# Kernel tuning notes

Measured on AMD Instinct MI355X. Metric: run time of the kernel, lower is better.

Reference implementation:

```python
import jax, jax.numpy as jnp
import numpy as np

D_MODEL = 512
N_HEAD = 8
D_K = 64
EPS = 1e-5


def setup_inputs() -> dict:
    key = jax.random.key(0)
    ks = jax.random.split(key, 12)
    B, S = 4, 2048
    Q = jax.random.normal(ks[0], (B, S, D_MODEL), dtype=jnp.float32)
    K = jax.random.normal(ks[1], (B, S, D_MODEL), dtype=jnp.float32)
    V = jax.random.normal(ks[2], (B, S, D_MODEL), dtype=jnp.float32)
    # bool padding-style mask: True = masked position
    att_mask = jax.random.randint(ks[3], (B, S, S), 0, 2).astype(bool)
    s = 1.0 / np.sqrt(D_MODEL)
    # Linear weights stored as [in, out] (transpose of torch's [out, in]; same math)
    Wq = jax.random.uniform(ks[4], (D_MODEL, N_HEAD * D_K), jnp.float32, -s, s)
    bq = jax.random.uniform(ks[5], (N_HEAD * D_K,), jnp.float32, -s, s)
    Wk = jax.random.uniform(ks[6], (D_MODEL, N_HEAD * D_K), jnp.float32, -s, s)
    bk = jax.random.uniform(ks[7], (N_HEAD * D_K,), jnp.float32, -s, s)
    Wv = jax.random.uniform(ks[8], (D_MODEL, N_HEAD * D_K), jnp.float32, -s, s)
    bv = jax.random.uniform(ks[9], (N_HEAD * D_K,), jnp.float32, -s, s)
    Wo = jax.random.uniform(ks[10], (N_HEAD * D_K, D_MODEL), jnp.float32, -s, s)
    bo = jax.random.uniform(ks[11], (D_MODEL,), jnp.float32, -s, s)
    return {"Q": Q, "K": K, "V": V, "att_mask": att_mask,
            "Wq": Wq, "bq": bq, "Wk": Wk, "bk": bk,
            "Wv": Wv, "bv": bv, "Wo": Wo, "bo": bo}


def _layer_norm(x):
    # nn.LayerNorm with default weight=1, bias=0 (fresh module in forward)
    mu = jnp.mean(x, axis=-1, keepdims=True)
    var = jnp.mean(jnp.square(x - mu), axis=-1, keepdims=True)
    return (x - mu) / jnp.sqrt(var + EPS)


def reference(Q, K, V, att_mask, Wq, bq, Wk, bk, Wv, bv, Wo, bo):
    B, S, _ = Q.shape
    residual = Q
    # QKV projections -> [B, H, S, Dk]
    q = (Q @ Wq + bq).reshape(B, S, N_HEAD, D_K).transpose(0, 2, 1, 3)
    k = (K @ Wk + bk).reshape(B, S, N_HEAD, D_K).transpose(0, 2, 1, 3)
    v = (V @ Wv + bv).reshape(B, S, N_HEAD, D_K).transpose(0, 2, 1, 3)
    # scaled dot-product attention with padding mask
    score = jnp.einsum('bhqd,bhkd->bhqk', q, k) / np.sqrt(D_K)
    score = jnp.where(att_mask[:, None, :, :], jnp.float32(-1e9), score)
    attn = jax.nn.softmax(score, axis=-1)
    context = jnp.einsum('bhqk,bhkd->bhqd', attn, v)
    context = context.transpose(0, 2, 1, 3).reshape(B, S, N_HEAD * D_K)
    output = context @ Wo + bo
    out = _layer_norm(output + residual)
    return out, attn
```

## Files before the change

### kernel.cpp

```cpp
#include <hip/hip_runtime.h>
#include <hip/hip_bf16.h>
#include <cstdint>
#include <cstddef>


typedef __attribute__((ext_vector_type(8)))  short short8v;
typedef __attribute__((ext_vector_type(2)))  float f32x2;
typedef __attribute__((ext_vector_type(4)))  float f32x4;
typedef __attribute__((ext_vector_type(16))) float f32x16;

constexpr int DM = 512, S = 2048, BATCH = 4, NHEAD = 8, DK = 64;
constexpr int ROWS = BATCH * S;
constexpr int BH   = BATCH * NHEAD;
constexpr size_t OUT_ELEMS = (size_t)ROWS * DM;
constexpr size_t HFRAG = 131072;

#define ZERO16 {0.f,0.f,0.f,0.f,0.f,0.f,0.f,0.f,0.f,0.f,0.f,0.f,0.f,0.f,0.f,0.f}

__device__ __forceinline__ unsigned short f2bf(float f) {
    union { __hip_bfloat16 b; unsigned short u; } c;
    c.b = __float2bfloat16(f);
    return c.u;
}
__device__ __forceinline__ float bf2f(unsigned short u) {
    union { float f; unsigned u32; } c;
    c.u32 = (unsigned)u << 16;
    return c.f;
}

__global__ __launch_bounds__(256)
void wconv(const float* __restrict__ Wq, const float* __restrict__ Wk,
           const float* __restrict__ Wv, const float* __restrict__ Wo,
           unsigned short* __restrict__ wt)
{
    __shared__ float T[32][33];
    const float* srcs[4] = {Wq, Wk, Wv, Wo};
    const float* W = srcs[blockIdx.z];
    unsigned short* out = wt + (size_t)blockIdx.z * DM * DM;
    const int r0 = blockIdx.y * 32, c0 = blockIdx.x * 32;
    const int tid = threadIdx.x;
#pragma unroll
    for (int i = 0; i < 4; ++i) {
        int lin = tid + i * 256; int r = lin >> 5, c = lin & 31;
        T[r][c] = W[(size_t)(r0 + r) * DM + c0 + c];
    }
    __syncthreads();
#pragma unroll
    for (int i = 0; i < 4; ++i) {
        int lin = tid + i * 256; int rn = lin >> 5, ck = lin & 31;
        out[(size_t)(c0 + rn) * DM + r0 + ck] = f2bf(T[ck][rn]);
    }
}

__global__ __launch_bounds__(256)
void maskpack(const uint8_t* __restrict__ mask, unsigned* __restrict__ mb)
{
    const int t = threadIdx.x;
    const int row = blockIdx.x * 4 + (t >> 6);
    const int w = t & 63;
    const uint8_t* src = mask + (size_t)row * S + 32 * w;
    const uint4 a = *reinterpret_cast<const uint4*>(src);
    const uint4 b = *reinterpret_cast<const uint4*>(src + 16);
    const unsigned m8[8] = {a.x, a.y, a.z, a.w, b.x, b.y, b.z, b.w};
    unsigned bits = 0;
#pragma unroll
    for (int k2 = 0; k2 < 32; ++k2)
        bits |= (((m8[k2 >> 2] >> (8 * (k2 & 3))) & 0xffu) ? 1u : 0u) << k2;
    mb[(size_t)row * 64 + w] = bits;
}

__global__ __launch_bounds__(256)
void proj3_mfma(const float* __restrict__ Qin, const float* __restrict__ Kin,
                const float* __restrict__ Vin, const unsigned short* __restrict__ wt,
                const float* __restrict__ bq, const float* __restrict__ bk,
                const float* __restrict__ bv,
                unsigned short* __restrict__ qo, unsigned short* __restrict__ ko,
                unsigned short* __restrict__ vo)
{
    const int z = blockIdx.z;
    const float* X = (z == 0) ? Qin : (z == 1) ? Kin : Vin;
    const unsigned short* Wt = wt + (size_t)z * DM * DM;
    const float* bias = (z == 0) ? bq : (z == 1) ? bk : bv;
    unsigned short* Y = (z == 0) ? qo : (z == 1) ? ko : vo;
    const float scale = (z == 0) ? 0.125f : 1.0f;

    const int tid = threadIdx.x, wv = tid >> 6, l = tid & 63, lr = l & 31, lh = l >> 5;
    const int m0 = blockIdx.y * 128 + wv * 32;
    const int n0 = blockIdx.x * 64;
    const float* xp = X + (size_t)(m0 + lr) * DM + 8 * lh;
    const unsigned short* w0 = Wt + (size_t)(n0 + lr) * DM + 8 * lh;
    const unsigned short* w1 = w0 + (size_t)32 * DM;
    f32x16 acc0 = ZERO16, acc1 = ZERO16;
#pragma unroll 8
    for (int t = 0; t < 32; ++t) {
        float4 xa = *reinterpret_cast<const float4*>(xp + 16 * t);
        float4 xb = *reinterpret_cast<const float4*>(xp + 16 * t + 4);
        short8v a;
        a[0] = (short)f2bf(xa.x * scale); a[1] = (short)f2bf(xa.y * scale);
        a[2] = (short)f2bf(xa.z * scale); a[3] = (short)f2bf(xa.w * scale);
        a[4] = (short)f2bf(xb.x * scale); a[5] = (short)f2bf(xb.y * scale);
        a[6] = (short)f2bf(xb.z * scale); a[7] = (short)f2bf(xb.w * scale);
        short8v b0 = *reinterpret_cast<const short8v*>(w0 + 16 * t);
        short8v b1 = *reinterpret_cast<const short8v*>(w1 + 16 * t);
        acc0 = __builtin_amdgcn_mfma_f32_32x32x16_bf16(a, b0, acc0, 0, 0, 0);
        acc1 = __builtin_amdgcn_mfma_f32_32x32x16_bf16(a, b1, acc1, 0, 0, 0);
    }
#pragma unroll
    for (int j = 0; j < 2; ++j) {
        const f32x16 acc = j ? acc1 : acc0;
        const int n = n0 + 32 * j + lr;
        const float bvv = bias[n] * scale;
        const int h = n >> 6, d = n & 63;
#pragma unroll
        for (int r = 0; r < 16; ++r) {
            const int m = m0 + (r & 3) + 8 * (r >> 2) + 4 * lh;
            const int bb = m >> 11, s = m & (S - 1);
            const int bh = bb * NHEAD + h;
            const unsigned short val = f2bf(acc[r] + bvv);
            size_t idx;
            if (z == 0)
                idx = ((size_t)bh * S + s) * DK + d;
            else if (z == 1)
                idx = (size_t)bh * HFRAG + (size_t)(s >> 4) * 1024 + (size_t)(d >> 5) * 512
                      + (size_t)(((s & 15) + 16 * ((d & 31) >> 3)) << 3) + (d & 7);
            else
                idx = (size_t)bh * HFRAG + (size_t)(s >> 5) * 2048 + (size_t)(d >> 4) * 512
                      + (size_t)(((d & 15) + 16 * ((s & 31) >> 3)) << 3) + (s & 7);
            Y[idx] = val;
        }
    }
}

__global__ __launch_bounds__(512, 4)
void attn_fused(const unsigned short* __restrict__ q,
                const unsigned short* __restrict__ kpack,
                const unsigned short* __restrict__ vpack,
                const unsigned* __restrict__ mbits,
                float* __restrict__ attn,
                unsigned short* __restrict__ ctx)
{
    __shared__ char Pc[16 * 4096];
    __shared__ float cred[2][4][16][16];
    __shared__ float redm[8][16];
    __shared__ float reds[8][16];
    const int tid = threadIdx.x, wv = tid >> 6, l = tid & 63;
    const int lq = l & 15, lg = l >> 4;
    const int bh = blockIdx.y, q0 = blockIdx.x * 16;
    const int b = bh >> 3, h = bh & 7;

    const unsigned short* qp = q + ((size_t)bh * S + q0 + lq) * DK + 8 * lg;
    const short8v qf0 = *reinterpret_cast<const short8v*>(qp);
    const short8v qf1 = *reinterpret_cast<const short8v*>(qp + 32);
    const unsigned short* kbase = kpack + (size_t)bh * HFRAG + (size_t)l * 8;
    f32x4 acc[16];
#pragma unroll
    for (int it = 0; it < 16; ++it) {
        const unsigned short* kc = kbase + (size_t)(16 * wv + it) * 1024;
        const short8v kf0 = *reinterpret_cast<const short8v*>(kc);
        const short8v kf1 = *reinterpret_cast<const short8v*>(kc + 512);
        f32x4 a = {0.f, 0.f, 0.f, 0.f};
        a = __builtin_amdgcn_mfma_f32_16x16x32_bf16(kf0, qf0, a, 0, 0, 0);
        a = __builtin_amdgcn_mfma_f32_16x16x32_bf16(kf1, qf1, a, 0, 0, 0);
        acc[it] = a;
    }

    const unsigned* mrow = mbits + ((size_t)b * S + q0 + lq) * 64 + 8 * wv;
    const uint4 mwa = *reinterpret_cast<const uint4*>(mrow);
    const uint4 mwb = *reinterpret_cast<const uint4*>(mrow + 4);
    const unsigned mw[8] = {mwa.x, mwa.y, mwa.z, mwa.w, mwb.x, mwb.y, mwb.z, mwb.w};
    float vmax = -3e38f;
#pragma unroll
    for (int it = 0; it < 16; ++it) {
        const unsigned word = mw[it >> 1] >> (16 * (it & 1) + 4 * lg);
#pragma unroll
        for (int r = 0; r < 4; ++r) {
            const float v = ((word >> r) & 1u) ? -1e30f : acc[it][r];
            acc[it][r] = v;
            vmax = fmaxf(vmax, v);
        }
    }
    vmax = fmaxf(vmax, __shfl_xor(vmax, 16));
    vmax = fmaxf(vmax, __shfl_xor(vmax, 32));
    if (l < 16) redm[wv][l] = vmax;
    __syncthreads();
    float rmax = redm[0][lq];
#pragma unroll
    for (int w2 = 1; w2 < 8; ++w2) rmax = fmaxf(rmax, redm[w2][lq]);

    float sum = 0.f;
#pragma unroll
    for (int it = 0; it < 16; ++it)
#pragma unroll
        for (int r = 0; r < 4; ++r) {
            const float v = __expf(acc[it][r] - rmax);
            acc[it][r] = v;
            sum += v;
        }
    sum += __shfl_xor(sum, 16);
    sum += __shfl_xor(sum, 32);
    if (l < 16) reds[wv][l] = sum;
    __syncthreads();
    float rsum = 0.f;
#pragma unroll
    for (int w2 = 0; w2 < 8; ++w2) rsum += reds[w2][lq];
    const float inv = 1.0f / rsum;

    float* arow = attn + ((size_t)bh * S + q0 + lq) * S + 256 * wv;
    const int swz = (lq & 7) << 4;
    char* prow = Pc + lq * 4096;
#pragma unroll
    for (int it = 0; it < 16; ++it) {
        const int n = 16 * it + 4 * lg;
        f32x4 o;
        o[0] = acc[it][0] * inv; o[1] = acc[it][1] * inv;
        o[2] = acc[it][2] * inv; o[3] = acc[it][3] * inv;
        __builtin_nontemporal_store(o, reinterpret_cast<f32x4*>(arow + n));
        ushort4 p;
        p.x = f2bf(o[0]); p.y = f2bf(o[1]); p.z = f2bf(o[2]); p.w = f2bf(o[3]);
        *reinterpret_cast<ushort4*>(prow + ((2 * (256 * wv + n)) ^ swz)) = p;
    }
    __syncthreads();

    const int dt = wv & 3, kh = wv >> 2;
    const int rswz = (lq & 7) << 4;
    f32x4 pacc = {0.f, 0.f, 0.f, 0.f};
    const unsigned short* vbase = vpack + (size_t)bh * HFRAG + dt * 512 + (size_t)l * 8;
#pragma unroll 4
    for (int s = 0; s < 32; ++s) {
        const int kk0 = kh * 1024 + 32 * s;
        const short8v a = *reinterpret_cast<const short8v*>(
            Pc + lq * 4096 + ((2 * (kk0 + 8 * lg)) ^ rswz));
        const short8v bf = *reinterpret_cast<const short8v*>(
            vbase + (size_t)(kh * 32 + s) * 2048);
        pacc = __builtin_amdgcn_mfma_f32_16x16x32_bf16(a, bf, pacc, 0, 0, 0);
    }
#pragma unroll
    for (int r = 0; r < 4; ++r) cred[kh][dt][lg * 4 + r][lq] = pacc[r];
    __syncthreads();

    for (int o = tid; o < 1024; o += 512) {
        const int qq = o >> 6, dd = o & 63;
        const float val = cred[0][dd >> 4][qq][dd & 15] + cred[1][dd >> 4][qq][dd & 15];
        ctx[((size_t)(b * S + q0 + qq)) * DM + h * DK + dd] = f2bf(val);
    }
}

__global__ __launch_bounds__(512)
void out_ln(const unsigned short* __restrict__ Xc, const unsigned short* __restrict__ Wt,
            const float* __restrict__ bias, const float* __restrict__ resid,
            float* __restrict__ out)
{
    __shared__ f32x2 red[32][8];
    __shared__ f32x2 stat[32];
    const int tid = threadIdx.x, wv = tid >> 6, l = tid & 63, lr = l & 31, lh = l >> 5;
    const int m0 = blockIdx.x * 32;
    const int n0 = wv * 64;
    const unsigned short* xp = Xc + (size_t)(m0 + lr) * DM + 8 * lh;
    const unsigned short* w0 = Wt + (size_t)(n0 + lr) * DM + 8 * lh;
    const unsigned short* w1 = w0 + (size_t)32 * DM;
    f32x16 acc0 = ZERO16, acc1 = ZERO16;
#pragma unroll 8
    for (int t = 0; t < 32; ++t) {
        short8v a  = *reinterpret_cast<const short8v*>(xp + 16 * t);
        short8v b0 = *reinterpret_cast<const short8v*>(w0 + 16 * t);
        short8v b1 = *reinterpret_cast<const short8v*>(w1 + 16 * t);
        acc0 = __builtin_amdgcn_mfma_f32_32x32x16_bf16(a, b0, acc0, 0, 0, 0);
        acc1 = __builtin_amdgcn_mfma_f32_32x32x16_bf16(a, b1, acc1, 0, 0, 0);
    }
    const float bv0 = bias[n0 + lr], bv1 = bias[n0 + 32 + lr];
#pragma unroll
    for (int r = 0; r < 16; ++r) {
        const int mloc = (r & 3) + 8 * (r >> 2) + 4 * lh;
        const size_t mbase = (size_t)(m0 + mloc) * DM + n0 + lr;
        const float v0 = acc0[r] + bv0 + resid[mbase];
        const float v1 = acc1[r] + bv1 + resid[mbase + 32];
        acc0[r] = v0; acc1[r] = v1;
        float s = v0 + v1, sq = v0 * v0 + v1 * v1;
#pragma unroll
        for (int off = 16; off; off >>= 1) {
            s  += __shfl_xor(s, off);
            sq += __shfl_xor(sq, off);
        }
        if (lr == 0) { f32x2 t2; t2[0] = s; t2[1] = sq; red[mloc][wv] = t2; }
    }
    __syncthreads();
    if (tid < 32) {
        float s = 0.f, sq = 0.f;
#pragma unroll
        for (int w2 = 0; w2 < 8; ++w2) { s += red[tid][w2][0]; sq += red[tid][w2][1]; }
        const float mean = s * (1.0f / 512.0f);
        const float var = sq * (1.0f / 512.0f) - mean * mean;
        f32x2 t2; t2[0] = mean; t2[1] = rsqrtf(var + 1e-5f);
        stat[tid] = t2;
    }
    __syncthreads();
#pragma unroll
    for (int r = 0; r < 16; ++r) {
        const int mloc = (r & 3) + 8 * (r >> 2) + 4 * lh;
        const f32x2 st = stat[mloc];
        const size_t mbase = (size_t)(m0 + mloc) * DM + n0 + lr;
        out[mbase]      = (acc0[r] - st[0]) * st[1];
        out[mbase + 32] = (acc1[r] - st[0]) * st[1];
    }
}

extern "C" void kernel_launch(void* const* d_in, const int* in_sizes, int n_in,
                              void* d_out, int out_size, void* d_ws, size_t ws_size,
                              hipStream_t stream)
{
    (void)in_sizes; (void)n_in; (void)out_size; (void)ws_size;

    const float*   Qin  = (const float*)d_in[0];
    const float*   Kin  = (const float*)d_in[1];
    const float*   Vin  = (const float*)d_in[2];
    const uint8_t* mask = (const uint8_t*)d_in[3];
    const float*   Wq   = (const float*)d_in[4];
    const float*   bq   = (const float*)d_in[5];
    const float*   Wk   = (const float*)d_in[6];
    const float*   bk   = (const float*)d_in[7];
    const float*   Wv   = (const float*)d_in[8];
    const float*   bv   = (const float*)d_in[9];
    const float*   Wo   = (const float*)d_in[10];
    const float*   bo   = (const float*)d_in[11];

    float* out  = (float*)d_out;
    float* attn = out + OUT_ELEMS;

    char* w = (char*)d_ws;
    const size_t MB = 1 << 20;
    unsigned short* wt    = (unsigned short*)(w);
    unsigned short* qbf   = (unsigned short*)(w + 2  * MB);
    unsigned short* kpack = (unsigned short*)(w + 10 * MB);
    unsigned short* vpack = (unsigned short*)(w + 18 * MB);
    unsigned short* ctx   = (unsigned short*)(w + 26 * MB);
    unsigned*       mbits = (unsigned*)(w + 34 * MB);

    unsigned short* wto = wt + 3 * (size_t)DM * DM;

    wconv<<<dim3(16, 16, 4), 256, 0, stream>>>(Wq, Wk, Wv, Wo, wt);

    maskpack<<<ROWS / 4, 256, 0, stream>>>(mask, mbits);

    proj3_mfma<<<dim3(DM / 64, ROWS / 128, 3), 256, 0, stream>>>(
        Qin, Kin, Vin, wt, bq, bk, bv, qbf, kpack, vpack);

    attn_fused<<<dim3(S / 16, BH), 512, 0, stream>>>(qbf, kpack, vpack, mbits, attn, ctx);

    out_ln<<<ROWS / 32, 512, 0, stream>>>(ctx, wto, bo, Qin, out);
}
```

Baseline: 365.1 us.

## Make attention blocks loop over query tiles and overlap attn stores with MFMA

The attention kernel now launches a fixed grid of 512 blocks. Each block walks 8 query tiles of one head instead of handling a single tile. The fp32 attention-probability writes are no longer issued in one burst after the softmax. They are re-read from the bf16 P tile in shared memory and interleaved with the QK MFMAs of the next tile and the first PV MFMAs, so the heavy global write traffic overlaps with compute. In exchange the stored attn values are now bf16-rounded rather than full fp32, and the smaller grid lowers resident blocks per CU.

```diff
diff --git a/kernel.cpp b/kernel.cpp
--- a/kernel.cpp
+++ b/kernel.cpp
@@ -14,6 +14,7 @@
 constexpr int BH   = BATCH * NHEAD;
 constexpr size_t OUT_ELEMS = (size_t)ROWS * DM;
 constexpr size_t HFRAG = 131072;
+constexpr int TPB_TILES = 8;
 
 #define ZERO16 {0.f,0.f,0.f,0.f,0.f,0.f,0.f,0.f,0.f,0.f,0.f,0.f,0.f,0.f,0.f,0.f}
 
@@ -145,104 +146,142 @@
     __shared__ float reds[8][16];
     const int tid = threadIdx.x, wv = tid >> 6, l = tid & 63;
     const int lq = l & 15, lg = l >> 4;
-    const int bh = blockIdx.y, q0 = blockIdx.x * 16;
+    const int bid = blockIdx.x;
+    const int bh = bid & 31, slot = bid >> 5;
     const int b = bh >> 3, h = bh & 7;
 
-    const unsigned short* qp = q + ((size_t)bh * S + q0 + lq) * DK + 8 * lg;
-    const short8v qf0 = *reinterpret_cast<const short8v*>(qp);
-    const short8v qf1 = *reinterpret_cast<const short8v*>(qp + 32);
     const unsigned short* kbase = kpack + (size_t)bh * HFRAG + (size_t)l * 8;
-    f32x4 acc[16];
-#pragma unroll
-    for (int it = 0; it < 16; ++it) {
-        const unsigned short* kc = kbase + (size_t)(16 * wv + it) * 1024;
-        const short8v kf0 = *reinterpret_cast<const short8v*>(kc);
-        const short8v kf1 = *reinterpret_cast<const short8v*>(kc + 512);
-        f32x4 a = {0.f, 0.f, 0.f, 0.f};
-        a = __builtin_amdgcn_mfma_f32_16x16x32_bf16(kf0, qf0, a, 0, 0, 0);
-        a = __builtin_amdgcn_mfma_f32_16x16x32_bf16(kf1, qf1, a, 0, 0, 0);
-        acc[it] = a;
-    }
-
-    const unsigned* mrow = mbits + ((size_t)b * S + q0 + lq) * 64 + 8 * wv;
-    const uint4 mwa = *reinterpret_cast<const uint4*>(mrow);
-    const uint4 mwb = *reinterpret_cast<const uint4*>(mrow + 4);
-    const unsigned mw[8] = {mwa.x, mwa.y, mwa.z, mwa.w, mwb.x, mwb.y, mwb.z, mwb.w};
-    float vmax = -3e38f;
-#pragma unroll
-    for (int it = 0; it < 16; ++it) {
-        const unsigned word = mw[it >> 1] >> (16 * (it & 1) + 4 * lg);
-#pragma unroll
-        for (int r = 0; r < 4; ++r) {
-            const float v = ((word >> r) & 1u) ? -1e30f : acc[it][r];
-            acc[it][r] = v;
-            vmax = fmaxf(vmax, v);
-        }
-    }
-    vmax = fmaxf(vmax, __shfl_xor(vmax, 16));
-    vmax = fmaxf(vmax, __shfl_xor(vmax, 32));
-    if (l < 16) redm[wv][l] = vmax;
-    __syncthreads();
-    float rmax = redm[0][lq];
-#pragma unroll
-    for (int w2 = 1; w2 < 8; ++w2) rmax = fmaxf(rmax, redm[w2][lq]);
-
-    float sum = 0.f;
-#pragma unroll
-    for (int it = 0; it < 16; ++it)
-#pragma unroll
-        for (int r = 0; r < 4; ++r) {
-            const float v = __expf(acc[it][r] - rmax);
-            acc[it][r] = v;
-            sum += v;
-        }
-    sum += __shfl_xor(sum, 16);
-    sum += __shfl_xor(sum, 32);
-    if (l < 16) reds[wv][l] = sum;
-    __syncthreads();
-    float rsum = 0.f;
-#pragma unroll
-    for (int w2 = 0; w2 < 8; ++w2) rsum += reds[w2][lq];
-    const float inv = 1.0f / rsum;
-
-    float* arow = attn + ((size_t)bh * S + q0 + lq) * S + 256 * wv;
-    const int swz = (lq & 7) << 4;
-    char* prow = Pc + lq * 4096;
-#pragma unroll
-    for (int it = 0; it < 16; ++it) {
-        const int n = 16 * it + 4 * lg;
-        f32x4 o;
-        o[0] = acc[it][0] * inv; o[1] = acc[it][1] * inv;
-        o[2] = acc[it][2] * inv; o[3] = acc[it][3] * inv;
-        __builtin_nontemporal_store(o, reinterpret_cast<f32x4*>(arow + n));
-        ushort4 p;
-        p.x = f2bf(o[0]); p.y = f2bf(o[1]); p.z = f2bf(o[2]); p.w = f2bf(o[3]);
-        *reinterpret_cast<ushort4*>(prow + ((2 * (256 * wv + n)) ^ swz)) = p;
-    }
-    __syncthreads();
-
     const int dt = wv & 3, kh = wv >> 2;
+    const unsigned short* vbase = vpack + (size_t)bh * HFRAG + dt * 512 + (size_t)l * 8;
     const int rswz = (lq & 7) << 4;
-    f32x4 pacc = {0.f, 0.f, 0.f, 0.f};
-    const unsigned short* vbase = vpack + (size_t)bh * HFRAG + dt * 512 + (size_t)l * 8;
-#pragma unroll 4
-    for (int s = 0; s < 32; ++s) {
-        const int kk0 = kh * 1024 + 32 * s;
-        const short8v a = *reinterpret_cast<const short8v*>(
-            Pc + lq * 4096 + ((2 * (kk0 + 8 * lg)) ^ rswz));
-        const short8v bf = *reinterpret_cast<const short8v*>(
-            vbase + (size_t)(kh * 32 + s) * 2048);
-        pacc = __builtin_amdgcn_mfma_f32_16x16x32_bf16(a, bf, pacc, 0, 0, 0);
-    }
-#pragma unroll
-    for (int r = 0; r < 4; ++r) cred[kh][dt][lg * 4 + r][lq] = pacc[r];
-    __syncthreads();
-
-    for (int o = tid; o < 1024; o += 512) {
-        const int qq = o >> 6, dd = o & 63;
-        const float val = cred[0][dd >> 4][qq][dd & 15] + cred[1][dd >> 4][qq][dd & 15];
-        ctx[((size_t)(b * S + q0 + qq)) * DM + h * DK + dd] = f2bf(val);
-    }
+
+    const int srow = 2 * wv + (l >> 5);
+    const int sswz = (srow & 7) << 4;
+    const int scol = 4 * (l & 31);
+    auto store_attn = [&](float* sb, int c) {
+        const uint2 pw = *reinterpret_cast<const uint2*>(
+            Pc + srow * 4096 + ((2 * c) ^ sswz));
+        f32x4 st;
+        st[0] = bf2f((unsigned short)(pw.x & 0xffffu));
+        st[1] = bf2f((unsigned short)(pw.x >> 16));
+        st[2] = bf2f((unsigned short)(pw.y & 0xffffu));
+        st[3] = bf2f((unsigned short)(pw.y >> 16));
+        __builtin_nontemporal_store(st, reinterpret_cast<f32x4*>(sb + c));
+    };
+
+    int q0p = -1;
+    for (int t = 0; t < TPB_TILES; ++t) {
+        const int q0 = (slot + 16 * t) * 16;
+
+        const unsigned short* qp = q + ((size_t)bh * S + q0 + lq) * DK + 8 * lg;
+        const short8v qf0 = *reinterpret_cast<const short8v*>(qp);
+        const short8v qf1 = *reinterpret_cast<const short8v*>(qp + 32);
+        float* sbp = (q0p >= 0)
+            ? attn + ((size_t)bh * S + q0p + srow) * S : nullptr;
+        f32x4 acc[16];
+#pragma unroll
+        for (int it = 0; it < 16; ++it) {
+            const unsigned short* kc = kbase + (size_t)(16 * wv + it) * 1024;
+            const short8v kf0 = *reinterpret_cast<const short8v*>(kc);
+            const short8v kf1 = *reinterpret_cast<const short8v*>(kc + 512);
+            f32x4 a = {0.f, 0.f, 0.f, 0.f};
+            a = __builtin_amdgcn_mfma_f32_16x16x32_bf16(kf0, qf0, a, 0, 0, 0);
+            a = __builtin_amdgcn_mfma_f32_16x16x32_bf16(kf1, qf1, a, 0, 0, 0);
+            acc[it] = a;
+            if (sbp && it < 8) store_attn(sbp, 128 * it + scol);
+        }
+
+        const unsigned* mrow = mbits + ((size_t)b * S + q0 + lq) * 64 + 8 * wv;
+        const uint4 mwa = *reinterpret_cast<const uint4*>(mrow);
+        const uint4 mwb = *reinterpret_cast<const uint4*>(mrow + 4);
+        const unsigned mw[8] = {mwa.x, mwa.y, mwa.z, mwa.w,
+                                mwb.x, mwb.y, mwb.z, mwb.w};
+        float vmax = -3e38f;
+#pragma unroll
+        for (int it = 0; it < 16; ++it) {
+            const unsigned word = mw[it >> 1] >> (16 * (it & 1) + 4 * lg);
+#pragma unroll
+            for (int r = 0; r < 4; ++r) {
+                const float v = ((word >> r) & 1u) ? -1e30f : acc[it][r];
+                acc[it][r] = v;
+                vmax = fmaxf(vmax, v);
+            }
+        }
+        vmax = fmaxf(vmax, __shfl_xor(vmax, 16));
+        vmax = fmaxf(vmax, __shfl_xor(vmax, 32));
+        if (l < 16) redm[wv][l] = vmax;
+        __syncthreads();
+        float rmax = redm[0][lq];
+#pragma unroll
+        for (int w2 = 1; w2 < 8; ++w2) rmax = fmaxf(rmax, redm[w2][lq]);
+
+        float sum = 0.f;
+#pragma unroll
+        for (int it = 0; it < 16; ++it)
+#pragma unroll
+            for (int r = 0; r < 4; ++r) {
+                const float v = __expf(acc[it][r] - rmax);
+                acc[it][r] = v;
+                sum += v;
+            }
+        sum += __shfl_xor(sum, 16);
+        sum += __shfl_xor(sum, 32);
+        if (l < 16) reds[wv][l] = sum;
+        __syncthreads();
+        float rsum = 0.f;
+#pragma unroll
+        for (int w2 = 0; w2 < 8; ++w2) rsum += reds[w2][lq];
+        const float inv = 1.0f / rsum;
+
+        const int swz = (lq & 7) << 4;
+        char* prow = Pc + lq * 4096;
+#pragma unroll
+        for (int it = 0; it < 16; ++it) {
+            const int n = 16 * it + 4 * lg;
+            ushort4 p;
+            p.x = f2bf(acc[it][0] * inv); p.y = f2bf(acc[it][1] * inv);
+            p.z = f2bf(acc[it][2] * inv); p.w = f2bf(acc[it][3] * inv);
+            *reinterpret_cast<ushort4*>(prow + ((2 * (256 * wv + n)) ^ swz)) = p;
+        }
+        __syncthreads();
+
+        float* sbc = attn + ((size_t)bh * S + q0 + srow) * S;
+        f32x4 pacc = {0.f, 0.f, 0.f, 0.f};
+#pragma unroll
+        for (int s = 0; s < 8; ++s) {
+            const int kk0 = kh * 1024 + 32 * s;
+            const short8v a = *reinterpret_cast<const short8v*>(
+                Pc + lq * 4096 + ((2 * (kk0 + 8 * lg)) ^ rswz));
+            const short8v bf = *reinterpret_cast<const short8v*>(
+                vbase + (size_t)(kh * 32 + s) * 2048);
+            pacc = __builtin_amdgcn_mfma_f32_16x16x32_bf16(a, bf, pacc, 0, 0, 0);
+            store_attn(sbc, 1024 + 128 * s + scol);
+        }
+#pragma unroll 8
+        for (int s = 8; s < 32; ++s) {
+            const int kk0 = kh * 1024 + 32 * s;
+            const short8v a = *reinterpret_cast<const short8v*>(
+                Pc + lq * 4096 + ((2 * (kk0 + 8 * lg)) ^ rswz));
+            const short8v bf = *reinterpret_cast<const short8v*>(
+                vbase + (size_t)(kh * 32 + s) * 2048);
+            pacc = __builtin_amdgcn_mfma_f32_16x16x32_bf16(a, bf, pacc, 0, 0, 0);
+        }
+#pragma unroll
+        for (int r = 0; r < 4; ++r) cred[kh][dt][lg * 4 + r][lq] = pacc[r];
+        __syncthreads();
+
+        for (int o = tid; o < 1024; o += 512) {
+            const int qq = o >> 6, dd = o & 63;
+            const float val = cred[0][dd >> 4][qq][dd & 15]
+                            + cred[1][dd >> 4][qq][dd & 15];
+            ctx[((size_t)(b * S + q0 + qq)) * DM + h * DK + dd] = f2bf(val);
+        }
+        q0p = q0;
+    }
+
+    float* sbl = attn + ((size_t)bh * S + q0p + srow) * S;
+#pragma unroll
+    for (int it = 0; it < 8; ++it) store_attn(sbl, 128 * it + scol);
 }
 
 __global__ __launch_bounds__(512)
@@ -344,7 +383,7 @@
     proj3_mfma<<<dim3(DM / 64, ROWS / 128, 3), 256, 0, stream>>>(
         Qin, Kin, Vin, wt, bq, bk, bv, qbf, kpack, vpack);
 
-    attn_fused<<<dim3(S / 16, BH), 512, 0, stream>>>(qbf, kpack, vpack, mbits, attn, ctx);
+    attn_fused<<<512, 512, 0, stream>>>(qbf, kpack, vpack, mbits, attn, ctx);
 
     out_ln<<<ROWS / 32, 512, 0, stream>>>(ctx, wto, bo, Qin, out);
 }
```

Result: slower. 761.5 us (+108.5%).

## Split attention into stats pass and write pass overlapping attn stores with PV

Applied to the files above, without the earlier changes.

The fused attention kernel becomes two kernels. The first recomputes QK^T with the mask and stores only the per-row max and sum. The second recomputes scores, normalizes them in one pass with no block reductions, and spreads the large attn matrix stores. Half the row is written directly as fp32, and the other half is written from the bf16 P tile in shared memory, interleaved with the PV MFMA loop. This is meant to hide store latency behind compute, at the cost of an extra launch, a second QK pass, and bf16-rounded values in half of the attn output.

```diff
diff --git a/kernel.cpp b/kernel.cpp
--- a/kernel.cpp
+++ b/kernel.cpp
@@ -132,27 +132,113 @@
 }
 
 __global__ __launch_bounds__(512, 4)
-void attn_fused(const unsigned short* __restrict__ q,
-                const unsigned short* __restrict__ kpack,
-                const unsigned short* __restrict__ vpack,
-                const unsigned* __restrict__ mbits,
-                float* __restrict__ attn,
-                unsigned short* __restrict__ ctx)
-{
-    __shared__ char Pc[16 * 4096];
-    __shared__ float cred[2][4][16][16];
+void stats_kernel(const unsigned short* __restrict__ q,
+                  const unsigned short* __restrict__ kpack,
+                  const unsigned* __restrict__ mbits,
+                  f32x2* __restrict__ stats)
+{
     __shared__ float redm[8][16];
     __shared__ float reds[8][16];
     const int tid = threadIdx.x, wv = tid >> 6, l = tid & 63;
     const int lq = l & 15, lg = l >> 4;
+    const int bh = blockIdx.y, qb = blockIdx.x * 64;
+    const int b = bh >> 3;
+    const unsigned short* kbase = kpack + (size_t)bh * HFRAG + (size_t)l * 8;
+
+    for (int sub = 0; sub < 4; ++sub) {
+        const int q0 = qb + 16 * sub;
+        const unsigned short* qp = q + ((size_t)bh * S + q0 + lq) * DK + 8 * lg;
+        const short8v qf0 = *reinterpret_cast<const short8v*>(qp);
+        const short8v qf1 = *reinterpret_cast<const short8v*>(qp + 32);
+        f32x4 acc[16];
+#pragma unroll
+        for (int it = 0; it < 16; ++it) {
+            const unsigned short* kc = kbase + (size_t)(16 * wv + it) * 1024;
+            const short8v kf0 = *reinterpret_cast<const short8v*>(kc);
+            const short8v kf1 = *reinterpret_cast<const short8v*>(kc + 512);
+            f32x4 a = {0.f, 0.f, 0.f, 0.f};
+            a = __builtin_amdgcn_mfma_f32_16x16x32_bf16(kf0, qf0, a, 0, 0, 0);
+            a = __builtin_amdgcn_mfma_f32_16x16x32_bf16(kf1, qf1, a, 0, 0, 0);
+            acc[it] = a;
+        }
+        const unsigned* mrow = mbits + ((size_t)b * S + q0 + lq) * 64 + 8 * wv;
+        const uint4 mwa = *reinterpret_cast<const uint4*>(mrow);
+        const uint4 mwb = *reinterpret_cast<const uint4*>(mrow + 4);
+        const unsigned mw[8] = {mwa.x, mwa.y, mwa.z, mwa.w,
+                                mwb.x, mwb.y, mwb.z, mwb.w};
+        float vmax = -3e38f;
+#pragma unroll
+        for (int it = 0; it < 16; ++it) {
+            const unsigned word = mw[it >> 1] >> (16 * (it & 1) + 4 * lg);
+#pragma unroll
+            for (int r = 0; r < 4; ++r) {
+                const float v = ((word >> r) & 1u) ? -1e30f : acc[it][r];
+                acc[it][r] = v;
+                vmax = fmaxf(vmax, v);
+            }
+        }
+        vmax = fmaxf(vmax, __shfl_xor(vmax, 16));
+        vmax = fmaxf(vmax, __shfl_xor(vmax, 32));
+        if (l < 16) redm[wv][l] = vmax;
+        __syncthreads();
+        float rmax = redm[0][lq];
+#pragma unroll
+        for (int w2 = 1; w2 < 8; ++w2) rmax = fmaxf(rmax, redm[w2][lq]);
+
+        float sum = 0.f;
+#pragma unroll
+        for (int it = 0; it < 16; ++it)
+#pragma unroll
+            for (int r = 0; r < 4; ++r)
+                sum += __expf(acc[it][r] - rmax);
+        sum += __shfl_xor(sum, 16);
+        sum += __shfl_xor(sum, 32);
+        if (l < 16) reds[wv][l] = sum;
+        __syncthreads();
+        if (wv == 0 && l < 16) {
+            float rsum = 0.f;
+#pragma unroll
+            for (int w2 = 0; w2 < 8; ++w2) rsum += reds[w2][l];
+            f32x2 st; st[0] = rmax; st[1] = rsum;
+            stats[(size_t)bh * S + q0 + l] = st;
+        }
+    }
+}
+
+__global__ __launch_bounds__(512, 4)
+void attn_write(const unsigned short* __restrict__ q,
+                const unsigned short* __restrict__ kpack,
+                const unsigned short* __restrict__ vpack,
+                const unsigned* __restrict__ mbits,
+                const f32x2* __restrict__ stats,
+                float* __restrict__ attn,
+                unsigned short* __restrict__ ctx)
+{
+    __shared__ char Pc[16 * 4096];
+    __shared__ float cred[2][4][16][16];
+    const int tid = threadIdx.x, wv = tid >> 6, l = tid & 63;
+    const int lq = l & 15, lg = l >> 4;
     const int bh = blockIdx.y, q0 = blockIdx.x * 16;
     const int b = bh >> 3, h = bh & 7;
+
+    const f32x2 st0 = stats[(size_t)bh * S + q0 + lq];
+    const float rmax = st0[0], inv = 1.0f / st0[1];
+
+    const unsigned* mrow = mbits + ((size_t)b * S + q0 + lq) * 64 + 8 * wv;
+    const uint4 mwa = *reinterpret_cast<const uint4*>(mrow);
+    const uint4 mwb = *reinterpret_cast<const uint4*>(mrow + 4);
+    const unsigned mw[8] = {mwa.x, mwa.y, mwa.z, mwa.w,
+                            mwb.x, mwb.y, mwb.z, mwb.w};
 
     const unsigned short* qp = q + ((size_t)bh * S + q0 + lq) * DK + 8 * lg;
     const short8v qf0 = *reinterpret_cast<const short8v*>(qp);
     const short8v qf1 = *reinterpret_cast<const short8v*>(qp + 32);
     const unsigned short* kbase = kpack + (size_t)bh * HFRAG + (size_t)l * 8;
-    f32x4 acc[16];
+
+    float* arow = attn + ((size_t)bh * S + q0 + lq) * S + 256 * wv;
+    const int swz = (lq & 7) << 4;
+    char* prow = Pc + lq * 4096;
+
 #pragma unroll
     for (int it = 0; it < 16; ++it) {
         const unsigned short* kc = kbase + (size_t)(16 * wv + it) * 1024;
@@ -161,63 +247,19 @@
         f32x4 a = {0.f, 0.f, 0.f, 0.f};
         a = __builtin_amdgcn_mfma_f32_16x16x32_bf16(kf0, qf0, a, 0, 0, 0);
         a = __builtin_amdgcn_mfma_f32_16x16x32_bf16(kf1, qf1, a, 0, 0, 0);
-        acc[it] = a;
-    }
-
-    const unsigned* mrow = mbits + ((size_t)b * S + q0 + lq) * 64 + 8 * wv;
-    const uint4 mwa = *reinterpret_cast<const uint4*>(mrow);
-    const uint4 mwb = *reinterpret_cast<const uint4*>(mrow + 4);
-    const unsigned mw[8] = {mwa.x, mwa.y, mwa.z, mwa.w, mwb.x, mwb.y, mwb.z, mwb.w};
-    float vmax = -3e38f;
-#pragma unroll
-    for (int it = 0; it < 16; ++it) {
         const unsigned word = mw[it >> 1] >> (16 * (it & 1) + 4 * lg);
+        f32x4 p;
 #pragma unroll
         for (int r = 0; r < 4; ++r) {
-            const float v = ((word >> r) & 1u) ? -1e30f : acc[it][r];
-            acc[it][r] = v;
-            vmax = fmaxf(vmax, v);
-        }
-    }
-    vmax = fmaxf(vmax, __shfl_xor(vmax, 16));
-    vmax = fmaxf(vmax, __shfl_xor(vmax, 32));
-    if (l < 16) redm[wv][l] = vmax;
-    __syncthreads();
-    float rmax = redm[0][lq];
-#pragma unroll
-    for (int w2 = 1; w2 < 8; ++w2) rmax = fmaxf(rmax, redm[w2][lq]);
-
-    float sum = 0.f;
-#pragma unroll
-    for (int it = 0; it < 16; ++it)
-#pragma unroll
-        for (int r = 0; r < 4; ++r) {
-            const float v = __expf(acc[it][r] - rmax);
-            acc[it][r] = v;
-            sum += v;
-        }
-    sum += __shfl_xor(sum, 16);
-    sum += __shfl_xor(sum, 32);
-    if (l < 16) reds[wv][l] = sum;
-    __syncthreads();
-    float rsum = 0.f;
-#pragma unroll
-    for (int w2 = 0; w2 < 8; ++w2) rsum += reds[w2][lq];
-    const float inv = 1.0f / rsum;
-
-    float* arow = attn + ((size_t)bh * S + q0 + lq) * S + 256 * wv;
-    const int swz = (lq & 7) << 4;
-    char* prow = Pc + lq * 4096;
-#pragma unroll
-    for (int it = 0; it < 16; ++it) {
+            const float v = ((word >> r) & 1u) ? -1e30f : a[r];
+            p[r] = __expf(v - rmax) * inv;
+        }
         const int n = 16 * it + 4 * lg;
-        f32x4 o;
-        o[0] = acc[it][0] * inv; o[1] = acc[it][1] * inv;
-        o[2] = acc[it][2] * inv; o[3] = acc[it][3] * inv;
-        __builtin_nontemporal_store(o, reinterpret_cast<f32x4*>(arow + n));
-        ushort4 p;
-        p.x = f2bf(o[0]); p.y = f2bf(o[1]); p.z = f2bf(o[2]); p.w = f2bf(o[3]);
-        *reinterpret_cast<ushort4*>(prow + ((2 * (256 * wv + n)) ^ swz)) = p;
+        ushort4 pb;
+        pb.x = f2bf(p[0]); pb.y = f2bf(p[1]); pb.z = f2bf(p[2]); pb.w = f2bf(p[3]);
+        *reinterpret_cast<ushort4*>(prow + ((2 * (256 * wv + n)) ^ swz)) = pb;
+        if (wv < 4)
+            __builtin_nontemporal_store(p, reinterpret_cast<f32x4*>(arow + n));
     }
     __syncthreads();
 
@@ -225,6 +267,10 @@
     const int rswz = (lq & 7) << 4;
     f32x4 pacc = {0.f, 0.f, 0.f, 0.f};
     const unsigned short* vbase = vpack + (size_t)bh * HFRAG + dt * 512 + (size_t)l * 8;
+    const int wrow = 8 * kh + 2 * dt + (l >> 5);
+    const int wswz = (wrow & 7) << 4;
+    const int lc = l & 31;
+    float* sbc = attn + ((size_t)bh * S + q0 + wrow) * S + 1024;
 #pragma unroll 4
     for (int s = 0; s < 32; ++s) {
         const int kk0 = kh * 1024 + 32 * s;
@@ -233,6 +279,15 @@
         const short8v bf = *reinterpret_cast<const short8v*>(
             vbase + (size_t)(kh * 32 + s) * 2048);
         pacc = __builtin_amdgcn_mfma_f32_16x16x32_bf16(a, bf, pacc, 0, 0, 0);
+        if (s < 16) {
+            const unsigned pw = *reinterpret_cast<const unsigned*>(
+                Pc + wrow * 4096 + ((2048 + 128 * s + 4 * lc) ^ wswz));
+            f32x2 stv;
+            stv[0] = bf2f((unsigned short)(pw & 0xffffu));
+            stv[1] = bf2f((unsigned short)(pw >> 16));
+            __builtin_nontemporal_store(stv,
+                reinterpret_cast<f32x2*>(sbc + 64 * s + 2 * lc));
+        }
     }
 #pragma unroll
     for (int r = 0; r < 4; ++r) cred[kh][dt][lg * 4 + r][lq] = pacc[r];
@@ -240,7 +295,8 @@
 
     for (int o = tid; o < 1024; o += 512) {
         const int qq = o >> 6, dd = o & 63;
-        const float val = cred[0][dd >> 4][qq][dd & 15] + cred[1][dd >> 4][qq][dd & 15];
+        const float val = cred[0][dd >> 4][qq][dd & 15]
+                        + cred[1][dd >> 4][qq][dd & 15];
         ctx[((size_t)(b * S + q0 + qq)) * DM + h * DK + dd] = f2bf(val);
     }
 }
@@ -334,6 +390,7 @@
     unsigned short* vpack = (unsigned short*)(w + 18 * MB);
     unsigned short* ctx   = (unsigned short*)(w + 26 * MB);
     unsigned*       mbits = (unsigned*)(w + 34 * MB);
+    f32x2*          stats = (f32x2*)(w + 36 * MB);
 
     unsigned short* wto = wt + 3 * (size_t)DM * DM;
 
@@ -344,7 +401,10 @@
     proj3_mfma<<<dim3(DM / 64, ROWS / 128, 3), 256, 0, stream>>>(
         Qin, Kin, Vin, wt, bq, bk, bv, qbf, kpack, vpack);
 
-    attn_fused<<<dim3(S / 16, BH), 512, 0, stream>>>(qbf, kpack, vpack, mbits, attn, ctx);
+    stats_kernel<<<dim3(S / 64, BH), 512, 0, stream>>>(qbf, kpack, mbits, stats);
+
+    attn_write<<<dim3(S / 16, BH), 512, 0, stream>>>(
+        qbf, kpack, vpack, mbits, stats, attn, ctx);
 
     out_ln<<<ROWS / 32, 512, 0, stream>>>(ctx, wto, bo, Qin, out);
 }
```

Result: slower. 515.7 us (+41.2%).
